# Kernel tuning notes

Hardware: AMD Instinct MI355X
Metric: run time of the kernel (lower is better)

Reference implementation:

```python
import jax, jax.numpy as jnp
import numpy as np

D_MODEL = 1024
N_HEADS = 16
D_K = D_MODEL // N_HEADS
B, S = 4, 2048


def setup_inputs() -> dict:
    key = jax.random.key(0)
    ks = jax.random.split(key, 9)
    sc = 1.0 / np.sqrt(D_MODEL)
    inp = {
        "x": jax.random.normal(ks[0], (B, S, D_MODEL), dtype=jnp.float32),
        # causal mask, broadcastable over batch and heads; 0 -> masked
        "mask": jnp.tril(jnp.ones((S, S), dtype=jnp.int32))[None, None, :, :],
        "Wq": jax.random.normal(ks[1], (D_MODEL, D_MODEL), dtype=jnp.float32) * sc,
        "bq": jax.random.normal(ks[2], (D_MODEL,), dtype=jnp.float32) * sc,
        "Wk": jax.random.normal(ks[3], (D_MODEL, D_MODEL), dtype=jnp.float32) * sc,
        "bk": jax.random.normal(ks[4], (D_MODEL,), dtype=jnp.float32) * sc,
        "Wv": jax.random.normal(ks[5], (D_MODEL, D_MODEL), dtype=jnp.float32) * sc,
        "bv": jax.random.normal(ks[6], (D_MODEL,), dtype=jnp.float32) * sc,
        "Wo": jax.random.normal(ks[7], (D_MODEL, D_MODEL), dtype=jnp.float32) * sc,
        "bo": jax.random.normal(ks[8], (D_MODEL,), dtype=jnp.float32) * sc,
    }
    return inp


def _split_heads(t):
    b, s, _ = t.shape
    return t.reshape(b, s, N_HEADS, D_K).transpose(0, 2, 1, 3)  # [B,H,S,dk]


def reference(x, mask, Wq, bq, Wk, bk, Wv, bv, Wo, bo):
    Q = _split_heads(x @ Wq.T + bq)
    K = _split_heads(x @ Wk.T + bk)
    V = _split_heads(x @ Wv.T + bv)
    scores = jnp.einsum("bhqd,bhkd->bhqk", Q, K) / jnp.sqrt(jnp.float32(D_K))
    scores = jnp.where(mask == 0, jnp.float32(-1e9), scores)
    weights = jax.nn.softmax(scores, axis=-1)
    attn = jnp.einsum("bhqk,bhkd->bhqd", weights, V)  # [B,H,S,dk]
    attn = attn.transpose(0, 2, 1, 3).reshape(x.shape[0], x.shape[1], D_MODEL)
    return attn @ Wo.T + bo
```

## Files before the change

kernel.cpp:

```cpp
#include <hip/hip_runtime.h>
#include <hip/hip_bf16.h>
#include <cstdint>

#define DM   1024
#define NH   16
#define DK   64
#define BB   4
#define SS   2048
#define MTOT (BB * SS)
#define PAD  68

typedef short short8 __attribute__((ext_vector_type(8)));
typedef float f32x4  __attribute__((ext_vector_type(4)));
using u16 = unsigned short;

__device__ inline u16 f2b(float f) {
    union { float f; unsigned int u; } v; v.f = f;
    unsigned int u = v.u;
    u += 0x7fffu + ((u >> 16) & 1u);
    return (u16)(u >> 16);
}
__device__ inline u16 f2b_trunc(float f) {
    union { float f; unsigned int u; } v; v.f = f;
    return (u16)(v.u >> 16);
}
__device__ inline float b2f(u16 s) {
    union { unsigned int u; float f; } v; v.u = ((unsigned int)s) << 16;
    return v.f;
}

__device__ inline void load_lds16(const u16* g, u16* l) {
    __builtin_amdgcn_global_load_lds(
        (const __attribute__((address_space(1))) unsigned int*)g,
        (__attribute__((address_space(3))) unsigned int*)l, 16, 0, 0);
}

struct CvtPtrs {
    const void *x, *Wq, *Wk, *Wv, *Wo, *bq, *bk, *bv, *bo;
    u16 *xb, *Wqb, *Wkb, *Wvb, *Wob, *bqb, *bkb, *bvb, *bob;
};

__global__ void convert_all(CvtPtrs p, int* __restrict__ flag)
{
    __shared__ int cnt;
    if (threadIdx.x == 0) cnt = 0;
    __syncthreads();
    int c = 0;
    for (int i = threadIdx.x; i < 512; i += 256) {
        const int e = (((const u16*)p.x)[i] >> 7) & 0xFF;
        if (e >= 100 && e <= 140) c++;
    }
    atomicAdd(&cnt, c);
    __syncthreads();
    const int isbf = (cnt >= 420) ? 1 : 0;
    if (blockIdx.x == 0 && threadIdx.x == 0) *flag = isbf;
    if (isbf) return;

    const size_t E  = (size_t)MTOT * DM;
    const size_t W1 = (size_t)DM * DM;
    const size_t i = ((size_t)blockIdx.x * blockDim.x + threadIdx.x) * 8;
    const float* s; u16* d; size_t off;
    if (i < E) {
        s = (const float*)p.x; d = p.xb; off = i;
    } else {
        size_t j = i - E;
        if (j < (W1 << 2)) {
            const int w = (int)(j >> 20); off = j & (W1 - 1);
            const float* ss[4] = {(const float*)p.Wq, (const float*)p.Wk,
                                  (const float*)p.Wv, (const float*)p.Wo};
            u16* dd[4] = {p.Wqb, p.Wkb, p.Wvb, p.Wob};
            s = ss[w]; d = dd[w];
        } else {
            j -= (W1 << 2);
            if (j >= 4 * DM) return;
            const int w = (int)(j >> 10); off = j & (DM - 1);
            const float* ss[4] = {(const float*)p.bq, (const float*)p.bk,
                                  (const float*)p.bv, (const float*)p.bo};
            u16* dd[4] = {p.bqb, p.bkb, p.bvb, p.bob};
            s = ss[w]; d = dd[w];
        }
    }
    const float4 f0 = *(const float4*)(s + off);
    const float4 f1 = *(const float4*)(s + off + 4);
    u16 tmp[8] = {f2b(f0.x), f2b(f0.y), f2b(f0.z), f2b(f0.w),
                  f2b(f1.x), f2b(f1.y), f2b(f1.z), f2b(f1.w)};
    *(int4*)(d + off) = *(const int4*)tmp;
}

__device__ __forceinline__
void gemm_body(const u16* __restrict__ A, const u16* __restrict__ Bw,
               const u16* __restrict__ bias, void* __restrict__ out,
               int mode, float scale, int isbf,
               u16 (*As)[64], u16 (*Bs)[64])
{
    const int tid  = threadIdx.x;
    const int wave = tid >> 6;
    const int lane = tid & 63;
    const int n0 = blockIdx.x * 128;
    const int m0 = blockIdx.y * 128;
    const int wm = (wave >> 1) * 64;
    const int wn = (wave & 1) * 64;

    const int lm   = lane & 15;
    const int quad = lane >> 4;
    const int kq   = quad * 8;
    const int rq   = quad * 4;

    const u16* gA = A  + (size_t)(m0 + 8*wave + (lane >> 3)) * DM + (lane & 7) * 8;
    const u16* gB = Bw + (size_t)(n0 + 8*wave + (lane >> 3)) * DM + (lane & 7) * 8;
    u16* ldsA = (u16*)((char*)&As[0][0] + wave * 1024);
    u16* ldsB = (u16*)((char*)&Bs[0][0] + wave * 1024);

    f32x4 acc[4][4] = {};

    for (int k0 = 0; k0 < DM; k0 += 64) {
        __syncthreads();
#pragma unroll
        for (int c = 0; c < 4; c++) {
            load_lds16(gA + (size_t)c*32*DM + k0, (u16*)((char*)ldsA + c*4096));
            load_lds16(gB + (size_t)c*32*DM + k0, (u16*)((char*)ldsB + c*4096));
        }
        __syncthreads();

#pragma unroll
        for (int ks = 0; ks < 2; ks++) {
            short8 af[4], bf[4];
#pragma unroll
            for (int i = 0; i < 4; i++) af[i] = *(const short8*)(&As[wm + 16*i + lm][ks*32 + kq]);
#pragma unroll
            for (int j = 0; j < 4; j++) bf[j] = *(const short8*)(&Bs[wn + 16*j + lm][ks*32 + kq]);
#pragma unroll
            for (int i = 0; i < 4; i++)
#pragma unroll
                for (int j = 0; j < 4; j++)
                    acc[i][j] = __builtin_amdgcn_mfma_f32_16x16x32_bf16(af[i], bf[j], acc[i][j], 0, 0, 0);
        }
    }

#pragma unroll
    for (int j = 0; j < 4; j++) {
        const int col = n0 + wn + 16*j + lm;
        const float bv = b2f(bias[col]);
        const int h = col >> 6, d = col & 63;
#pragma unroll
        for (int i = 0; i < 4; i++) {
            if (mode == 2) {
                const int row0 = m0 + wm + 16*i + rq;
                const int b = row0 >> 11, s = row0 & 2047;
                u16 tmp[4];
#pragma unroll
                for (int r = 0; r < 4; r++)
                    tmp[r] = f2b((acc[i][j][r] + bv) * scale);
                const size_t idx = (((size_t)(b*NH + h) * DK) + d) * SS + s;
                *(uint2*)(&((u16*)out)[idx]) = *(const uint2*)tmp;
            } else {
#pragma unroll
                for (int r = 0; r < 4; r++) {
                    const int row = m0 + wm + 16*i + rq + r;
                    const float v = (acc[i][j][r] + bv) * scale;
                    if (mode == 0) {
                        const size_t idx = (size_t)row * DM + col;
                        if (isbf) ((u16*)out)[idx] = f2b(v);
                        else      ((float*)out)[idx] = v;
                    } else {
                        const int b = row >> 11, s = row & 2047;
                        const size_t idx = (((size_t)(b*NH + h) * SS) + s) * DK + d;
                        ((u16*)out)[idx] = f2b(v);
                    }
                }
            }
        }
    }
}

__global__ __launch_bounds__(256)
void gemm_qkv(CvtPtrs p, u16* __restrict__ Qb, u16* __restrict__ Kb,
              u16* __restrict__ Vb, float qscale, const int* __restrict__ flag)
{
    __shared__ __align__(16) u16 As[128][64];
    __shared__ __align__(16) u16 Bs[128][64];
    const int isbf = *flag;
    const u16* A = isbf ? (const u16*)p.x : p.xb;
    const int z = blockIdx.z;
    const u16* Bw, *bias; u16* out;
    if (z == 0)      { Bw = isbf ? (const u16*)p.Wq : p.Wqb; bias = isbf ? (const u16*)p.bq : p.bqb; out = Qb; }
    else if (z == 1) { Bw = isbf ? (const u16*)p.Wk : p.Wkb; bias = isbf ? (const u16*)p.bk : p.bkb; out = Kb; }
    else             { Bw = isbf ? (const u16*)p.Wv : p.Wvb; bias = isbf ? (const u16*)p.bv : p.bvb; out = Vb; }
    const int mode  = (z == 2) ? 2 : 1;
    const float sc  = (z == 0) ? qscale : 1.0f;
    gemm_body(A, Bw, bias, out, mode, sc, 1, As, Bs);
}

__global__ __launch_bounds__(256)
void gemm_out(const u16* __restrict__ Ab, CvtPtrs p, void* __restrict__ out,
              const int* __restrict__ flag)
{
    __shared__ __align__(16) u16 As[128][64];
    __shared__ __align__(16) u16 Bs[128][64];
    const int isbf = *flag;
    const u16* Bw   = isbf ? (const u16*)p.Wo : p.Wob;
    const u16* bias = isbf ? (const u16*)p.bo : p.bob;
    gemm_body(Ab, Bw, bias, out, 0, 1.0f, isbf, As, Bs);
}

__global__ __launch_bounds__(256)
void attn_causal(const u16* __restrict__ Q, const u16* __restrict__ K,
                 const u16* __restrict__ VT, u16* __restrict__ O)
{
    __shared__ __align__(16) u16 Ks[2][64][PAD];
    __shared__ __align__(16) u16 Vs[2][64][PAD];
    __shared__ __align__(16) u16 Ps[128][PAD];

    const int tid  = threadIdx.x;
    const int wave = tid >> 6;
    const int lane = tid & 63;
    const int qx = blockIdx.x;
    const int h = blockIdx.y, b = blockIdx.z;
    const int bh = b * NH + h;

    const u16* Kg = K  + (size_t)bh * SS * DK;
    const u16* Vg = VT + (size_t)bh * DK * SS;

    const int srow = tid >> 3;
    const int scol = (tid & 7) * 8;
    const int lm = lane & 15, quad = lane >> 4, kq = quad * 8, rq = quad * 4;

#pragma unroll
    for (int seg = 0; seg < 2; seg++) {
        const int qt = seg ? (15 - qx) : qx;
        const int q0 = qt * 128;
        const int nt = 2 * (qt + 1);
        const u16* Qg = Q + ((size_t)bh * SS + q0) * DK;

        short8 qa[2][2];
#pragma unroll
        for (int mi = 0; mi < 2; mi++)
#pragma unroll
            for (int ks = 0; ks < 2; ks++)
                qa[mi][ks] = *(const short8*)(&Qg[(size_t)(32*wave + 16*mi + lm) * DK + ks*32 + kq]);

        int4 kv0 = *(const int4*)(&Kg[(size_t)srow * DK + scol]);
        int4 kv1 = *(const int4*)(&Kg[(size_t)(srow + 32) * DK + scol]);
        int4 vv0 = *(const int4*)(&Vg[(size_t)srow * SS + scol]);
        int4 vv1 = *(const int4*)(&Vg[(size_t)(srow + 32) * SS + scol]);
        *(int4*)(&Ks[0][srow][scol])      = kv0;
        *(int4*)(&Ks[0][srow + 32][scol]) = kv1;
        *(int4*)(&Vs[0][srow][scol])      = vv0;
        *(int4*)(&Vs[0][srow + 32][scol]) = vv1;
        __syncthreads();

        kv0 = *(const int4*)(&Kg[(size_t)(64 + srow) * DK + scol]);
        kv1 = *(const int4*)(&Kg[(size_t)(64 + srow + 32) * DK + scol]);
        vv0 = *(const int4*)(&Vg[(size_t)srow * SS + 64 + scol]);
        vv1 = *(const int4*)(&Vg[(size_t)(srow + 32) * SS + 64 + scol]);

        f32x4 o[2][4] = {};
        float lacc[2][4] = {};

        for (int t = 0; t < nt; t++) {
            const int buf = t & 1;
            const int k0 = 64 * t;

            f32x4 sc[2][4] = {};
#pragma unroll
            for (int ks = 0; ks < 2; ks++)
#pragma unroll
                for (int j = 0; j < 4; j++) {
                    const short8 bfr = *(const short8*)(&Ks[buf][16*j + lm][ks*32 + kq]);
                    sc[0][j] = __builtin_amdgcn_mfma_f32_16x16x32_bf16(qa[0][ks], bfr, sc[0][j], 0, 0, 0);
                    sc[1][j] = __builtin_amdgcn_mfma_f32_16x16x32_bf16(qa[1][ks], bfr, sc[1][j], 0, 0, 0);
                }

            if (k0 + 63 > q0 + 32*wave) {
#pragma unroll
                for (int mi = 0; mi < 2; mi++)
#pragma unroll
                    for (int j = 0; j < 4; j++)
#pragma unroll
                        for (int r = 0; r < 4; r++)
                            if (k0 + 16*j + lm > q0 + 32*wave + 16*mi + rq + r)
                                sc[mi][j][r] = -1e30f;
            }

#pragma unroll
            for (int mi = 0; mi < 2; mi++)
#pragma unroll
                for (int j = 0; j < 4; j++)
#pragma unroll
                    for (int r = 0; r < 4; r++) {
                        const float pv = __builtin_amdgcn_exp2f(sc[mi][j][r]);
                        lacc[mi][r] += pv;
                        Ps[32*wave + 16*mi + rq + r][16*j + lm] = f2b_trunc(pv);
                    }

#pragma unroll
            for (int ks = 0; ks < 2; ks++) {
                const short8 pa0 = *(const short8*)(&Ps[32*wave + lm][ks*32 + kq]);
                const short8 pa1 = *(const short8*)(&Ps[32*wave + 16 + lm][ks*32 + kq]);
#pragma unroll
                for (int j = 0; j < 4; j++) {
                    const short8 vfr = *(const short8*)(&Vs[buf][16*j + lm][ks*32 + kq]);
                    o[0][j] = __builtin_amdgcn_mfma_f32_16x16x32_bf16(pa0, vfr, o[0][j], 0, 0, 0);
                    o[1][j] = __builtin_amdgcn_mfma_f32_16x16x32_bf16(pa1, vfr, o[1][j], 0, 0, 0);
                }
            }

            if (t + 1 < nt) {
                const int nb = buf ^ 1;
                *(int4*)(&Ks[nb][srow][scol])      = kv0;
                *(int4*)(&Ks[nb][srow + 32][scol]) = kv1;
                *(int4*)(&Vs[nb][srow][scol])      = vv0;
                *(int4*)(&Vs[nb][srow + 32][scol]) = vv1;
                if (t + 2 < nt) {
                    const int kn = 64 * (t + 2);
                    kv0 = *(const int4*)(&Kg[(size_t)(kn + srow) * DK + scol]);
                    kv1 = *(const int4*)(&Kg[(size_t)(kn + srow + 32) * DK + scol]);
                    vv0 = *(const int4*)(&Vg[(size_t)srow * SS + kn + scol]);
                    vv1 = *(const int4*)(&Vg[(size_t)(srow + 32) * SS + kn + scol]);
                }
            }
            __syncthreads();
        }

#pragma unroll
        for (int mi = 0; mi < 2; mi++)
#pragma unroll
            for (int r = 0; r < 4; r++) {
                float v = lacc[mi][r];
#pragma unroll
                for (int off = 1; off < 16; off <<= 1)
                    v += __shfl_xor(v, off, 64);
                const float inv = 1.f / v;
                const size_t rowg = (size_t)b * SS + q0 + 32*wave + 16*mi + rq + r;
#pragma unroll
                for (int j = 0; j < 4; j++)
                    O[rowg * DM + h*DK + 16*j + lm] = f2b(o[mi][j][r] * inv);
            }
    }
}

extern "C" void kernel_launch(void* const* d_in, const int* in_sizes, int n_in,
                              void* d_out, int out_size, void* d_ws, size_t ws_size,
                              hipStream_t stream)
{
    (void)in_sizes; (void)n_in; (void)out_size; (void)ws_size;

    int* flag = (int*)d_ws;
    u16* ws = (u16*)((char*)d_ws + 16);

    const size_t E  = (size_t)MTOT * DM;
    const size_t W1 = (size_t)DM * DM;
    u16* xb  = ws;
    u16* Wqb = ws + E;
    u16* Wkb = Wqb + W1;
    u16* Wvb = Wkb + W1;
    u16* Wob = Wvb + W1;
    u16* bqb = Wob + W1;
    u16* bkb = bqb + DM;
    u16* bvb = bkb + DM;
    u16* bob = bvb + DM;
    u16* Qb  = bob + DM;
    u16* Kb  = Qb + E;
    u16* Vb  = Kb + E;
    u16* Ab  = xb;

    CvtPtrs p;
    p.x = d_in[0];
    p.Wq = d_in[2]; p.bq = d_in[3];
    p.Wk = d_in[4]; p.bk = d_in[5];
    p.Wv = d_in[6]; p.bv = d_in[7];
    p.Wo = d_in[8]; p.bo = d_in[9];
    p.xb = xb;
    p.Wqb = Wqb; p.Wkb = Wkb; p.Wvb = Wvb; p.Wob = Wob;
    p.bqb = bqb; p.bkb = bkb; p.bvb = bvb; p.bob = bob;

    const int cvt_blocks = (int)((E + 4*W1 + 4*DM) / 2048);
    convert_all<<<cvt_blocks, 256, 0, stream>>>(p, flag);

    const float qscale = 0.18033688011112042f;

    gemm_qkv<<<dim3(DM/128, MTOT/128, 3), 256, 0, stream>>>(
        p, Qb, Kb, Vb, qscale, flag);
    attn_causal<<<dim3(SS/256, NH, BB), 256, 0, stream>>>(Qb, Kb, Vb, Ab);
    gemm_out<<<dim3(DM/128, MTOT/128), 256, 0, stream>>>(Ab, p, d_out, flag);
}
```

Before: 315.9 us.

## XOR-swizzle GEMM LDS tiles and remap blocks for XCD-local L2 reuse

The GEMM loader now permutes the 16-byte chunk each lane fetches from global memory with an XOR of the row index, so the LDS tile is stored swizzled. The MFMA fragment reads apply the same XOR, which is meant to remove LDS bank conflicts on the unpadded 64-wide rows. Both GEMM launches also switch to a 1D grid whose block ids are decoded so that each XCD (id & 7) handles a contiguous set of M rows, keeping the A tiles it shares in its own L2. The cost is a little extra index arithmetic, plus grid sizes that are now hardcoded to these exact shapes.

Result: faster. 294.6 us (-6.8%).

```diff
diff --git a/kernel.cpp b/kernel.cpp
--- a/kernel.cpp
+++ b/kernel.cpp
@@ -90,14 +90,12 @@
 __device__ __forceinline__
 void gemm_body(const u16* __restrict__ A, const u16* __restrict__ Bw,
                const u16* __restrict__ bias, void* __restrict__ out,
-               int mode, float scale, int isbf,
+               int mode, float scale, int isbf, int m0, int n0,
                u16 (*As)[64], u16 (*Bs)[64])
 {
     const int tid  = threadIdx.x;
     const int wave = tid >> 6;
     const int lane = tid & 63;
-    const int n0 = blockIdx.x * 128;
-    const int m0 = blockIdx.y * 128;
     const int wm = (wave >> 1) * 64;
     const int wn = (wave & 1) * 64;
 
@@ -106,8 +104,10 @@
     const int kq   = quad * 8;
     const int rq   = quad * 4;
 
-    const u16* gA = A  + (size_t)(m0 + 8*wave + (lane >> 3)) * DM + (lane & 7) * 8;
-    const u16* gB = Bw + (size_t)(n0 + 8*wave + (lane >> 3)) * DM + (lane & 7) * 8;
+    const int lrow   = lane >> 3;
+    const int lchunk = (lane & 7) ^ lrow;
+    const u16* gA = A  + (size_t)(m0 + 8*wave + lrow) * DM + lchunk * 8;
+    const u16* gB = Bw + (size_t)(n0 + 8*wave + lrow) * DM + lchunk * 8;
     u16* ldsA = (u16*)((char*)&As[0][0] + wave * 1024);
     u16* ldsB = (u16*)((char*)&Bs[0][0] + wave * 1024);
 
@@ -124,11 +124,12 @@
 
 #pragma unroll
         for (int ks = 0; ks < 2; ks++) {
+            const int ca = ((ks*4 + quad) ^ (lm & 7)) * 8;
             short8 af[4], bf[4];
 #pragma unroll
-            for (int i = 0; i < 4; i++) af[i] = *(const short8*)(&As[wm + 16*i + lm][ks*32 + kq]);
-#pragma unroll
-            for (int j = 0; j < 4; j++) bf[j] = *(const short8*)(&Bs[wn + 16*j + lm][ks*32 + kq]);
+            for (int i = 0; i < 4; i++) af[i] = *(const short8*)(&As[wm + 16*i + lm][ca]);
+#pragma unroll
+            for (int j = 0; j < 4; j++) bf[j] = *(const short8*)(&Bs[wn + 16*j + lm][ca]);
 #pragma unroll
             for (int i = 0; i < 4; i++)
 #pragma unroll
@@ -179,16 +180,21 @@
 {
     __shared__ __align__(16) u16 As[128][64];
     __shared__ __align__(16) u16 Bs[128][64];
+    const int id  = blockIdx.x;
+    const int xcd = id & 7;
+    const int j   = id >> 3;
+    const int m0  = (xcd * 8 + (j & 7)) * 128;
+    const int n0  = ((j >> 3) & 7) * 128;
+    const int z   = j >> 6;
     const int isbf = *flag;
     const u16* A = isbf ? (const u16*)p.x : p.xb;
-    const int z = blockIdx.z;
     const u16* Bw, *bias; u16* out;
     if (z == 0)      { Bw = isbf ? (const u16*)p.Wq : p.Wqb; bias = isbf ? (const u16*)p.bq : p.bqb; out = Qb; }
     else if (z == 1) { Bw = isbf ? (const u16*)p.Wk : p.Wkb; bias = isbf ? (const u16*)p.bk : p.bkb; out = Kb; }
     else             { Bw = isbf ? (const u16*)p.Wv : p.Wvb; bias = isbf ? (const u16*)p.bv : p.bvb; out = Vb; }
     const int mode  = (z == 2) ? 2 : 1;
     const float sc  = (z == 0) ? qscale : 1.0f;
-    gemm_body(A, Bw, bias, out, mode, sc, 1, As, Bs);
+    gemm_body(A, Bw, bias, out, mode, sc, 1, m0, n0, As, Bs);
 }
 
 __global__ __launch_bounds__(256)
@@ -197,10 +203,15 @@
 {
     __shared__ __align__(16) u16 As[128][64];
     __shared__ __align__(16) u16 Bs[128][64];
+    const int id  = blockIdx.x;
+    const int xcd = id & 7;
+    const int j   = id >> 3;
+    const int m0  = (xcd * 8 + (j & 7)) * 128;
+    const int n0  = (j >> 3) * 128;
     const int isbf = *flag;
     const u16* Bw   = isbf ? (const u16*)p.Wo : p.Wob;
     const u16* bias = isbf ? (const u16*)p.bo : p.bob;
-    gemm_body(Ab, Bw, bias, out, 0, 1.0f, isbf, As, Bs);
+    gemm_body(Ab, Bw, bias, out, 0, 1.0f, isbf, m0, n0, As, Bs);
 }
 
 __global__ __launch_bounds__(256)
@@ -379,8 +390,7 @@
 
     const float qscale = 0.18033688011112042f;
 
-    gemm_qkv<<<dim3(DM/128, MTOT/128, 3), 256, 0, stream>>>(
-        p, Qb, Kb, Vb, qscale, flag);
+    gemm_qkv<<<1536, 256, 0, stream>>>(p, Qb, Kb, Vb, qscale, flag);
     attn_causal<<<dim3(SS/256, NH, BB), 256, 0, stream>>>(Qb, Kb, Vb, Ab);
-    gemm_out<<<dim3(DM/128, MTOT/128), 256, 0, stream>>>(Ab, p, d_out, flag);
-}
+    gemm_out<<<512, 256, 0, stream>>>(Ab, p, d_out, flag);
+}
```
